# Kernel tuning notes

Measured on AMD Instinct MI355X. Metric: run time of the kernel, lower is better.

Reference implementation:

```python
import jax, jax.numpy as jnp
import numpy as np

D_MODEL = 1024
N_HEADS = 16
D_K = D_MODEL // N_HEADS
SEQ = 4096
BATCH = 1
THETA = 10000.0


def setup_inputs() -> dict:
    key = jax.random.key(0)
    ks = jax.random.split(key, 5)
    scale = 0.02
    x = jax.random.normal(ks[0], (BATCH, SEQ, D_MODEL), dtype=jnp.float32)
    token_positions = jnp.broadcast_to(jnp.arange(SEQ, dtype=jnp.int64 if jax.config.jax_enable_x64 else jnp.int32)[None, :], (BATCH, SEQ))
    Wq = jax.random.normal(ks[1], (D_MODEL, D_MODEL), dtype=jnp.float32) * scale
    Wk = jax.random.normal(ks[2], (D_MODEL, D_MODEL), dtype=jnp.float32) * scale
    Wv = jax.random.normal(ks[3], (D_MODEL, D_MODEL), dtype=jnp.float32) * scale
    Wo = jax.random.normal(ks[4], (D_MODEL, D_MODEL), dtype=jnp.float32) * scale
    return {"x": x, "token_positions": token_positions, "Wq": Wq, "Wk": Wk, "Wv": Wv, "Wo": Wo}


def _apply_rope(t, token_positions, theta=THETA):
    # t: (b, h, s, d_k); token_positions: (b, s)
    d_k = t.shape[-1]
    inv_freq = theta ** (-jnp.arange(0, d_k, 2, dtype=jnp.float32) / d_k)  # (d_k/2,)
    ang = token_positions.astype(jnp.float32)[:, :, None] * inv_freq  # (b, s, d_k/2)
    cos = jnp.cos(ang)[:, None, :, :]  # (b, 1, s, d_k/2)
    sin = jnp.sin(ang)[:, None, :, :]
    te, to = t[..., 0::2], t[..., 1::2]
    re = te * cos - to * sin
    ro = te * sin + to * cos
    # interleave back: (..., d_k/2, 2) -> (..., d_k)
    return jnp.stack([re, ro], axis=-1).reshape(t.shape)


def reference(x, token_positions, Wq, Wk, Wv, Wo):
    b, s, d_model = x.shape
    h, d_k = N_HEADS, D_K
    q = (x @ Wq.T).reshape(b, s, h, d_k).transpose(0, 2, 1, 3)  # (b,h,s,d_k)
    k = (x @ Wk.T).reshape(b, s, h, d_k).transpose(0, 2, 1, 3)
    v = (x @ Wv.T).reshape(b, s, h, d_k).transpose(0, 2, 1, 3)
    q = _apply_rope(q, token_positions)
    k = _apply_rope(k, token_positions)
    scores = jnp.einsum('bhqd,bhkd->bhqk', q, k) / jnp.sqrt(jnp.float32(d_k))
    causal = jnp.tril(jnp.ones((s, s), dtype=bool))[None, None]
    scores = jnp.where(causal, scores, jnp.float32(-1e9))
    attn = jax.nn.softmax(scores, axis=-1)
    out = jnp.einsum('bhqk,bhkd->bhqd', attn, v)  # (b,h,s,d_k)
    out = out.transpose(0, 2, 1, 3).reshape(b, s, d_model)
    return out @ Wo.T
```

## Files before the change

kernel.cpp:

```cpp
#include <hip/hip_runtime.h>
#include <hip/hip_bf16.h>
#include <math.h>


#define SEQ 4096
#define DM  1024
#define NH  16
#define DK  64

typedef __attribute__((ext_vector_type(8))) short short8;
typedef __attribute__((ext_vector_type(4))) float floatx4;

static __device__ __forceinline__ short f2bf(float f) {
    __hip_bfloat16 h = __float2bfloat16(f);
    return __builtin_bit_cast(short, h);
}

static __device__ __forceinline__ short8 load8_f32_as_bf16(const float* p) {
    float4 a = *reinterpret_cast<const float4*>(p);
    float4 b = *reinterpret_cast<const float4*>(p + 4);
    short8 s;
    s[0] = f2bf(a.x); s[1] = f2bf(a.y); s[2] = f2bf(a.z); s[3] = f2bf(a.w);
    s[4] = f2bf(b.x); s[5] = f2bf(b.y); s[6] = f2bf(b.z); s[7] = f2bf(b.w);
    return s;
}

static __device__ __forceinline__ void gl2lds16(const __hip_bfloat16* g, short* l) {
    __builtin_amdgcn_global_load_lds(
        (const __attribute__((address_space(1))) unsigned int*)g,
        (__attribute__((address_space(3))) unsigned int*)l, 16, 0, 0);
}

static __device__ __forceinline__ int read_pos(const int* tp32, int s) {
    return (tp32[1] == 1) ? tp32[s] : tp32[2 * s];
}

__global__ __launch_bounds__(256) void cvt_kernel(
    const float* __restrict__ src, __hip_bfloat16* __restrict__ dst, int n8)
{
    int i = blockIdx.x * blockDim.x + threadIdx.x;
    if (i < n8) {
        short8 v = load8_f32_as_bf16(src + (size_t)i * 8);
        *reinterpret_cast<short8*>((short*)dst + (size_t)i * 8) = v;
    }
}

__global__ __launch_bounds__(256) void rope_tab_kernel(
    const int* __restrict__ tp, float2* __restrict__ tab)
{
    int idx = blockIdx.x * blockDim.x + threadIdx.x;
    if (idx < SEQ * 32) {
        int s = idx >> 5, pair = idx & 31;
        float inv_freq = exp2f(-(float)(2 * pair) * (13.287712379549449f / 64.f));
        float sn, cs;
        sincosf((float)read_pos(tp, s) * inv_freq, &sn, &cs);
        tab[idx] = make_float2(cs, sn);
    }
}

__global__ __launch_bounds__(256) void qkv_rope_kernel(
    const __hip_bfloat16* __restrict__ xb,
    const float2* __restrict__ tab,
    const __hip_bfloat16* __restrict__ Wqb,
    const __hip_bfloat16* __restrict__ Wkb,
    const __hip_bfloat16* __restrict__ Wvb,
    __hip_bfloat16* __restrict__ q_ws,
    __hip_bfloat16* __restrict__ k_ws,
    __hip_bfloat16* __restrict__ vt_ws)
{
    __shared__ __align__(16) short pool[17408];
    short* As = pool;
    short* Bs = pool + 8192;

    const int by = blockIdx.y;
    const int wsel = by >> 3;
    const __hip_bfloat16* W = (wsel == 0) ? Wqb : (wsel == 1 ? Wkb : Wvb);
    const int nloc0 = (by & 7) * 128;
    const int m0 = blockIdx.x * 128;

    const int t = threadIdx.x;
    const int lane = t & 63;
    const int w = t >> 6;
    const int quad = lane >> 4;
    const int ln = lane & 15;
    const int wm = (w >> 1) * 64;
    const int wn = (w & 1) * 64;

    floatx4 acc[4][4];
    #pragma unroll
    for (int i = 0; i < 4; i++)
        #pragma unroll
        for (int j = 0; j < 4; j++) acc[i][j] = (floatx4){0.f, 0.f, 0.f, 0.f};

    for (int k0 = 0; k0 < DM; k0 += 64) {
        #pragma unroll
        for (int it = 0; it < 4; it++) {
            int row = w * 32 + it * 8 + (lane >> 3);
            int sg = (lane & 7) ^ (row & 7);
            gl2lds16(&xb[(size_t)(m0 + row) * DM + k0 + sg * 8], &As[(w * 32 + it * 8) * 64]);
            gl2lds16(&W[(size_t)(nloc0 + row) * DM + k0 + sg * 8], &Bs[(w * 32 + it * 8) * 64]);
        }
        __syncthreads();

        short8 af[4][2], bfr[4][2];
        #pragma unroll
        for (int i = 0; i < 4; i++)
            #pragma unroll
            for (int kc = 0; kc < 2; kc++)
                af[i][kc] = *reinterpret_cast<const short8*>(
                    &As[(wm + i * 16 + ln) * 64 + (((kc * 4 + quad) ^ (ln & 7)) << 3)]);
        #pragma unroll
        for (int j = 0; j < 4; j++)
            #pragma unroll
            for (int kc = 0; kc < 2; kc++)
                bfr[j][kc] = *reinterpret_cast<const short8*>(
                    &Bs[(wn + j * 16 + ln) * 64 + (((kc * 4 + quad) ^ (ln & 7)) << 3)]);

        #pragma unroll
        for (int kc = 0; kc < 2; kc++)
            #pragma unroll
            for (int i = 0; i < 4; i++)
                #pragma unroll
                for (int j = 0; j < 4; j++)
                    acc[i][j] = __builtin_amdgcn_mfma_f32_16x16x32_bf16(
                        af[i][kc], bfr[j][kc], acc[i][j], 0, 0, 0);
        __syncthreads();
    }

    if (wsel < 2) {
        __hip_bfloat16* dst = (wsel == 0) ? q_ws : k_ws;
        const float qscale = (wsel == 0) ? 0.125f : 1.0f;
        #pragma unroll
        for (int j = 0; j < 4; j++) {
            int cnl = wn + j * 16 + ln;
            int pair = ((nloc0 + cnl) & 63) >> 1;
            #pragma unroll
            for (int i = 0; i < 4; i++) {
                int rowl = wm + i * 16 + quad * 4;
                #pragma unroll
                for (int r = 0; r < 4; r++) {
                    float2 t2 = tab[(size_t)(m0 + rowl + r) * 32 + pair];
                    float val = acc[i][j][r];
                    float partner = __shfl_xor(val, 1, 64);
                    float res = val * t2.x + (((lane & 1) ? partner : -partner) * t2.y);
                    pool[(rowl + r) * 136 + cnl] = f2bf(res * qscale);
                }
            }
        }
        __syncthreads();
        int row = t >> 1, half = t & 1;
        size_t gbase = (size_t)(m0 + row) * DM + nloc0 + half * 64;
        #pragma unroll
        for (int c = 0; c < 8; c++)
            *reinterpret_cast<short8*>(&dst[gbase + c * 8]) =
                *reinterpret_cast<const short8*>(&pool[row * 136 + half * 64 + c * 8]);
    } else {
        #pragma unroll
        for (int j = 0; j < 4; j++) {
            int cnl = wn + j * 16 + ln;
            #pragma unroll
            for (int i = 0; i < 4; i++) {
                int s0 = wm + i * 16 + quad * 4;
                #pragma unroll
                for (int r = 0; r < 4; r++)
                    pool[cnl * 136 + s0 + r] = f2bf(acc[i][j][r]);
            }
        }
        __syncthreads();
        int cnl = t >> 1, sh = t & 1;
        size_t base = (size_t)(nloc0 + cnl) * SEQ + m0 + sh * 64;
        #pragma unroll
        for (int c = 0; c < 8; c++)
            *reinterpret_cast<short8*>(&vt_ws[base + c * 8]) =
                *reinterpret_cast<const short8*>(&pool[cnl * 136 + sh * 64 + c * 8]);
    }
}

__global__ __launch_bounds__(512) void attn_kernel(
    const __hip_bfloat16* __restrict__ q_ws,
    const __hip_bfloat16* __restrict__ k_ws,
    const __hip_bfloat16* __restrict__ vt_ws,
    __hip_bfloat16* __restrict__ o_ws)
{
    __shared__ __align__(16) short Kt[2][64 * 64];
    __shared__ __align__(16) short Vt[2][64 * 64];
    __shared__ short P[8][16 * 72];

    const int head = blockIdx.y;
    const int bx = blockIdx.x;
    const int qbA0 = (31 - bx) * 128;
    const int qbB0 = bx * 128;
    const int t = threadIdx.x;
    const int lane = t & 63;
    const int w = t >> 6;
    const int quad = lane >> 4;
    const int ln = lane & 15;
    const int niter = qbA0 / 64 + 2;

    const int qAbase = qbA0 + w * 16;
    const int qBbase = qbB0 + w * 16;

    const int keyl = w * 8 + (lane >> 3);
    const int sg = (lane & 7) ^ (keyl & 7);

    auto stage = [&](int b, int kb) {
        gl2lds16(&k_ws[(size_t)(kb + keyl) * DM + head * 64 + sg * 8], &Kt[b][w * 512]);
        gl2lds16(&vt_ws[(size_t)(head * 64 + keyl) * SEQ + kb + sg * 8], &Vt[b][w * 512]);
    };

    short8 qfA[2], qfB[2];
    #pragma unroll
    for (int kk = 0; kk < 2; kk++) {
        qfA[kk] = *reinterpret_cast<const short8*>(
            &q_ws[(size_t)(qAbase + ln) * DM + head * 64 + kk * 32 + quad * 8]);
        qfB[kk] = *reinterpret_cast<const short8*>(
            &q_ws[(size_t)(qBbase + ln) * DM + head * 64 + kk * 32 + quad * 8]);
    }

    floatx4 accA[4], accB[4];
    float lA[4] = {0.f, 0.f, 0.f, 0.f}, lB[4] = {0.f, 0.f, 0.f, 0.f};
    #pragma unroll
    for (int nt = 0; nt < 4; nt++) {
        accA[nt] = (floatx4){0.f, 0.f, 0.f, 0.f};
        accB[nt] = (floatx4){0.f, 0.f, 0.f, 0.f};
    }
    const floatx4 zero4 = {0.f, 0.f, 0.f, 0.f};

    stage(0, 0);
    int buf = 0;
    for (int it = 0; it < niter; it++) {
        const int kb = it * 64;
        __syncthreads();
        if (it + 1 < niter) stage(buf ^ 1, kb + 64);

        short8 kf[4][2], vf[4][2];
        #pragma unroll
        for (int nt = 0; nt < 4; nt++)
            #pragma unroll
            for (int kk = 0; kk < 2; kk++) {
                kf[nt][kk] = *reinterpret_cast<const short8*>(
                    &Kt[buf][(nt * 16 + ln) * 64 + (((kk * 4 + quad) ^ (ln & 7)) << 3)]);
                vf[nt][kk] = *reinterpret_cast<const short8*>(
                    &Vt[buf][(nt * 16 + ln) * 64 + (((kk * 4 + quad) ^ (ln & 7)) << 3)]);
            }

        if (kb <= qAbase + 15) {
            floatx4 sacc[4];
            #pragma unroll
            for (int nt = 0; nt < 4; nt++) {
                floatx4 s = __builtin_amdgcn_mfma_f32_16x16x32_bf16(qfA[0], kf[nt][0], zero4, 0, 0, 0);
                sacc[nt] = __builtin_amdgcn_mfma_f32_16x16x32_bf16(qfA[1], kf[nt][1], s, 0, 0, 0);
            }
            if (kb + 63 > qAbase) {
                #pragma unroll
                for (int nt = 0; nt < 4; nt++) {
                    int kpos = kb + nt * 16 + ln;
                    #pragma unroll
                    for (int r = 0; r < 4; r++)
                        if (kpos > qAbase + quad * 4 + r) sacc[nt][r] = -1e9f;
                }
            }
            #pragma unroll
            for (int nt = 0; nt < 4; nt++)
                #pragma unroll
                for (int r = 0; r < 4; r++) {
                    float p = __expf(sacc[nt][r]);
                    sacc[nt][r] = p;
                    lA[r] += p;
                }
            #pragma unroll
            for (int nt = 0; nt < 4; nt++)
                #pragma unroll
                for (int r = 0; r < 4; r++)
                    P[w][(quad * 4 + r) * 72 + nt * 16 + ln] = f2bf(sacc[nt][r]);
            short8 pa[2];
            #pragma unroll
            for (int kk = 0; kk < 2; kk++)
                pa[kk] = *reinterpret_cast<const short8*>(&P[w][ln * 72 + kk * 32 + quad * 8]);
            #pragma unroll
            for (int nt = 0; nt < 4; nt++) {
                floatx4 o = __builtin_amdgcn_mfma_f32_16x16x32_bf16(pa[0], vf[nt][0], accA[nt], 0, 0, 0);
                accA[nt] = __builtin_amdgcn_mfma_f32_16x16x32_bf16(pa[1], vf[nt][1], o, 0, 0, 0);
            }
        }
        if (kb <= qBbase + 15) {
            floatx4 sacc[4];
            #pragma unroll
            for (int nt = 0; nt < 4; nt++) {
                floatx4 s = __builtin_amdgcn_mfma_f32_16x16x32_bf16(qfB[0], kf[nt][0], zero4, 0, 0, 0);
                sacc[nt] = __builtin_amdgcn_mfma_f32_16x16x32_bf16(qfB[1], kf[nt][1], s, 0, 0, 0);
            }
            if (kb + 63 > qBbase) {
                #pragma unroll
                for (int nt = 0; nt < 4; nt++) {
                    int kpos = kb + nt * 16 + ln;
                    #pragma unroll
                    for (int r = 0; r < 4; r++)
                        if (kpos > qBbase + quad * 4 + r) sacc[nt][r] = -1e9f;
                }
            }
            #pragma unroll
            for (int nt = 0; nt < 4; nt++)
                #pragma unroll
                for (int r = 0; r < 4; r++) {
                    float p = __expf(sacc[nt][r]);
                    sacc[nt][r] = p;
                    lB[r] += p;
                }
            #pragma unroll
            for (int nt = 0; nt < 4; nt++)
                #pragma unroll
                for (int r = 0; r < 4; r++)
                    P[w][(quad * 4 + r) * 72 + nt * 16 + ln] = f2bf(sacc[nt][r]);
            short8 pa[2];
            #pragma unroll
            for (int kk = 0; kk < 2; kk++)
                pa[kk] = *reinterpret_cast<const short8*>(&P[w][ln * 72 + kk * 32 + quad * 8]);
            #pragma unroll
            for (int nt = 0; nt < 4; nt++) {
                floatx4 o = __builtin_amdgcn_mfma_f32_16x16x32_bf16(pa[0], vf[nt][0], accB[nt], 0, 0, 0);
                accB[nt] = __builtin_amdgcn_mfma_f32_16x16x32_bf16(pa[1], vf[nt][1], o, 0, 0, 0);
            }
        }
        buf ^= 1;
    }

    #pragma unroll
    for (int r = 0; r < 4; r++) {
        float l = lA[r];
        #pragma unroll
        for (int off = 1; off < 16; off <<= 1)
            l += __shfl_xor(l, off, 64);
        float rl = 1.f / l;
        int row = qAbase + quad * 4 + r;
        #pragma unroll
        for (int nt = 0; nt < 4; nt++)
            o_ws[(size_t)row * DM + head * 64 + nt * 16 + ln] =
                __float2bfloat16(accA[nt][r] * rl);
    }
    #pragma unroll
    for (int r = 0; r < 4; r++) {
        float l = lB[r];
        #pragma unroll
        for (int off = 1; off < 16; off <<= 1)
            l += __shfl_xor(l, off, 64);
        float rl = 1.f / l;
        int row = qBbase + quad * 4 + r;
        #pragma unroll
        for (int nt = 0; nt < 4; nt++)
            o_ws[(size_t)row * DM + head * 64 + nt * 16 + ln] =
                __float2bfloat16(accB[nt][r] * rl);
    }
}

__global__ __launch_bounds__(256) void oproj_kernel(
    const __hip_bfloat16* __restrict__ o_in,
    const float* __restrict__ Wo,
    float* __restrict__ out)
{
    __shared__ __align__(16) char smem[33792];
    short* As = (short*)smem;
    short* Bs = As + 8192;
    float* fpool = (float*)smem;

    const int m0 = blockIdx.x * 128;
    const int n0 = blockIdx.y * 128;

    const int t = threadIdx.x;
    const int lane = t & 63;
    const int w = t >> 6;
    const int quad = lane >> 4;
    const int ln = lane & 15;
    const int wm = (w >> 1) * 64;
    const int wn = (w & 1) * 64;

    floatx4 acc[4][4];
    #pragma unroll
    for (int i = 0; i < 4; i++)
        #pragma unroll
        for (int j = 0; j < 4; j++) acc[i][j] = (floatx4){0.f, 0.f, 0.f, 0.f};

    for (int k0 = 0; k0 < DM; k0 += 64) {
        #pragma unroll
        for (int it = 0; it < 4; it++) {
            int row = w * 32 + it * 8 + (lane >> 3);
            int sg = (lane & 7) ^ (row & 7);
            gl2lds16(&o_in[(size_t)(m0 + row) * DM + k0 + sg * 8], &As[(w * 32 + it * 8) * 64]);
        }
        #pragma unroll
        for (int p = 0; p < 4; p++) {
            int r = (t >> 3) + p * 32;
            int sg = t & 7;
            *reinterpret_cast<short8*>(&Bs[r * 64 + ((sg ^ (r & 7)) << 3)]) =
                load8_f32_as_bf16(&Wo[(size_t)(n0 + r) * DM + k0 + sg * 8]);
        }
        __syncthreads();

        short8 af[4][2], bfr[4][2];
        #pragma unroll
        for (int i = 0; i < 4; i++)
            #pragma unroll
            for (int kc = 0; kc < 2; kc++)
                af[i][kc] = *reinterpret_cast<const short8*>(
                    &As[(wm + i * 16 + ln) * 64 + (((kc * 4 + quad) ^ (ln & 7)) << 3)]);
        #pragma unroll
        for (int j = 0; j < 4; j++)
            #pragma unroll
            for (int kc = 0; kc < 2; kc++)
                bfr[j][kc] = *reinterpret_cast<const short8*>(
                    &Bs[(wn + j * 16 + ln) * 64 + (((kc * 4 + quad) ^ (ln & 7)) << 3)]);

        #pragma unroll
        for (int kc = 0; kc < 2; kc++)
            #pragma unroll
            for (int i = 0; i < 4; i++)
                #pragma unroll
                for (int j = 0; j < 4; j++)
                    acc[i][j] = __builtin_amdgcn_mfma_f32_16x16x32_bf16(
                        af[i][kc], bfr[j][kc], acc[i][j], 0, 0, 0);
        __syncthreads();
    }

    #pragma unroll
    for (int ph = 0; ph < 2; ph++) {
        if ((w >> 1) == ph) {
            #pragma unroll
            for (int j = 0; j < 4; j++)
                #pragma unroll
                for (int i = 0; i < 4; i++) {
                    int rl = i * 16 + quad * 4;
                    #pragma unroll
                    for (int r = 0; r < 4; r++)
                        fpool[(rl + r) * 132 + wn + j * 16 + ln] = acc[i][j][r];
                }
        }
        __syncthreads();
        int row = t >> 2;
        int c0 = (t & 3) * 32;
        size_t gbase = (size_t)(m0 + ph * 64 + row) * DM + n0 + c0;
        #pragma unroll
        for (int c = 0; c < 8; c++)
            *reinterpret_cast<float4*>(&out[gbase + c * 4]) =
                *reinterpret_cast<const float4*>(&fpool[row * 132 + c0 + c * 4]);
        __syncthreads();
    }
}

extern "C" void kernel_launch(void* const* d_in, const int* in_sizes, int n_in,
                              void* d_out, int out_size, void* d_ws, size_t ws_size,
                              hipStream_t stream) {
    const float* x  = (const float*)d_in[0];
    const int* tp   = (const int*)d_in[1];
    const float* Wq = (const float*)d_in[2];
    const float* Wk = (const float*)d_in[3];
    const float* Wv = (const float*)d_in[4];
    const float* Wo = (const float*)d_in[5];
    float* out = (float*)d_out;

    char* ws = (char*)d_ws;
    const size_t MB = 1024 * 1024;
    __hip_bfloat16* xb    = (__hip_bfloat16*)(ws);
    __hip_bfloat16* q_ws  = (__hip_bfloat16*)(ws + 8  * MB);
    __hip_bfloat16* k_ws  = (__hip_bfloat16*)(ws + 16 * MB);
    __hip_bfloat16* vt_ws = (__hip_bfloat16*)(ws + 24 * MB);
    __hip_bfloat16* o_ws  = xb;
    __hip_bfloat16* Wqb = (__hip_bfloat16*)d_out;
    __hip_bfloat16* Wkb = Wqb + (size_t)DM * DM;
    __hip_bfloat16* Wvb = Wkb + (size_t)DM * DM;
    float2* tab = (float2*)((char*)d_out + 6 * MB);

    cvt_kernel<<<2048, 256, 0, stream>>>(x,  xb,  (SEQ * DM) / 8);
    cvt_kernel<<<512,  256, 0, stream>>>(Wq, Wqb, (DM * DM) / 8);
    cvt_kernel<<<512,  256, 0, stream>>>(Wk, Wkb, (DM * DM) / 8);
    cvt_kernel<<<512,  256, 0, stream>>>(Wv, Wvb, (DM * DM) / 8);
    rope_tab_kernel<<<(SEQ * 32 + 255) / 256, 256, 0, stream>>>(tp, tab);

    qkv_rope_kernel<<<dim3(32, 24), 256, 0, stream>>>(xb, tab, Wqb, Wkb, Wvb, q_ws, k_ws, vt_ws);
    attn_kernel<<<dim3(16, 16), 512, 0, stream>>>(q_ws, k_ws, vt_ws, o_ws);
    oproj_kernel<<<dim3(32, 8), 256, 0, stream>>>(o_ws, Wo, out);
}
```

Baseline: 252.4 us.

## Fuse prep launches and transpose attention score MFMA for packed P stores

Merges the four fp32-to-bf16 conversion launches and the RoPE table launch into a single prep kernel, removing four kernel launches and their inter-launch gaps. In the attention kernel, the score MFMA operands are swapped so each lane holds four consecutive keys for one query. This allows P to be written to shared memory as packed 4-element stores into an XOR-swizzled, unpadded layout, and reduces the row-sum to one scalar per lane. The risk is a different LDS bank pattern and some extra shuffles in the epilogue.

Result: faster. 235.1 us (-6.9%).

```diff
diff --git a/kernel.cpp b/kernel.cpp
--- a/kernel.cpp
+++ b/kernel.cpp
@@ -10,6 +10,7 @@
 
 typedef __attribute__((ext_vector_type(8))) short short8;
 typedef __attribute__((ext_vector_type(4))) float floatx4;
+typedef __attribute__((ext_vector_type(4))) short short4v;
 
 static __device__ __forceinline__ short f2bf(float f) {
     __hip_bfloat16 h = __float2bfloat16(f);
@@ -35,26 +36,33 @@
     return (tp32[1] == 1) ? tp32[s] : tp32[2 * s];
 }
 
-__global__ __launch_bounds__(256) void cvt_kernel(
-    const float* __restrict__ src, __hip_bfloat16* __restrict__ dst, int n8)
+__global__ __launch_bounds__(256) void prep_kernel(
+    const float* __restrict__ x,  const float* __restrict__ Wq,
+    const float* __restrict__ Wk, const float* __restrict__ Wv,
+    const int* __restrict__ tp,
+    __hip_bfloat16* __restrict__ xb,  __hip_bfloat16* __restrict__ Wqb,
+    __hip_bfloat16* __restrict__ Wkb, __hip_bfloat16* __restrict__ Wvb,
+    float2* __restrict__ tab)
 {
-    int i = blockIdx.x * blockDim.x + threadIdx.x;
-    if (i < n8) {
-        short8 v = load8_f32_as_bf16(src + (size_t)i * 8);
-        *reinterpret_cast<short8*>((short*)dst + (size_t)i * 8) = v;
-    }
-}
-
-__global__ __launch_bounds__(256) void rope_tab_kernel(
-    const int* __restrict__ tp, float2* __restrict__ tab)
-{
-    int idx = blockIdx.x * blockDim.x + threadIdx.x;
-    if (idx < SEQ * 32) {
-        int s = idx >> 5, pair = idx & 31;
-        float inv_freq = exp2f(-(float)(2 * pair) * (13.287712379549449f / 64.f));
-        float sn, cs;
-        sincosf((float)read_pos(tp, s) * inv_freq, &sn, &cs);
-        tab[idx] = make_float2(cs, sn);
+    int b = blockIdx.x;
+    if (b < 3584) {
+        const float* src; __hip_bfloat16* dst; int off;
+        if (b < 2048)      { src = x;  dst = xb;  off = b; }
+        else if (b < 2560) { src = Wq; dst = Wqb; off = b - 2048; }
+        else if (b < 3072) { src = Wk; dst = Wkb; off = b - 2560; }
+        else               { src = Wv; dst = Wvb; off = b - 3072; }
+        size_t i = (size_t)off * 256 + threadIdx.x;
+        short8 v = load8_f32_as_bf16(src + i * 8);
+        *reinterpret_cast<short8*>((short*)dst + i * 8) = v;
+    } else {
+        int idx = (b - 3584) * 256 + threadIdx.x;
+        if (idx < SEQ * 32) {
+            int s = idx >> 5, pair = idx & 31;
+            float inv_freq = exp2f(-(float)(2 * pair) * (13.287712379549449f / 64.f));
+            float sn, cs;
+            sincosf((float)read_pos(tp, s) * inv_freq, &sn, &cs);
+            tab[idx] = make_float2(cs, sn);
+        }
     }
 }
 
@@ -184,7 +192,7 @@
 {
     __shared__ __align__(16) short Kt[2][64 * 64];
     __shared__ __align__(16) short Vt[2][64 * 64];
-    __shared__ short P[8][16 * 72];
+    __shared__ __align__(16) short P[8][16 * 64];
 
     const int head = blockIdx.y;
     const int bx = blockIdx.x;
@@ -195,10 +203,11 @@
     const int w = t >> 6;
     const int quad = lane >> 4;
     const int ln = lane & 15;
-    const int niter = qbA0 / 64 + 2;
+    const int niter = (31 - bx) * 2 + 2;
 
     const int qAbase = qbA0 + w * 16;
     const int qBbase = qbB0 + w * 16;
+    const int e = ((ln & 7) << 1) ^ (ln & 8);
 
     const int keyl = w * 8 + (lane >> 3);
     const int sg = (lane & 7) ^ (keyl & 7);
@@ -218,7 +227,7 @@
     }
 
     floatx4 accA[4], accB[4];
-    float lA[4] = {0.f, 0.f, 0.f, 0.f}, lB[4] = {0.f, 0.f, 0.f, 0.f};
+    float lA = 0.f, lB = 0.f;
     #pragma unroll
     for (int nt = 0; nt < 4; nt++) {
         accA[nt] = (floatx4){0.f, 0.f, 0.f, 0.f};
@@ -248,16 +257,17 @@
             floatx4 sacc[4];
             #pragma unroll
             for (int nt = 0; nt < 4; nt++) {
-                floatx4 s = __builtin_amdgcn_mfma_f32_16x16x32_bf16(qfA[0], kf[nt][0], zero4, 0, 0, 0);
-                sacc[nt] = __builtin_amdgcn_mfma_f32_16x16x32_bf16(qfA[1], kf[nt][1], s, 0, 0, 0);
-            }
+                floatx4 s = __builtin_amdgcn_mfma_f32_16x16x32_bf16(kf[nt][0], qfA[0], zero4, 0, 0, 0);
+                sacc[nt] = __builtin_amdgcn_mfma_f32_16x16x32_bf16(kf[nt][1], qfA[1], s, 0, 0, 0);
+            }
+            const int qpos = qAbase + ln;
             if (kb + 63 > qAbase) {
                 #pragma unroll
                 for (int nt = 0; nt < 4; nt++) {
-                    int kpos = kb + nt * 16 + ln;
+                    int kbase = kb + nt * 16 + quad * 4;
                     #pragma unroll
                     for (int r = 0; r < 4; r++)
-                        if (kpos > qAbase + quad * 4 + r) sacc[nt][r] = -1e9f;
+                        if (kbase + r > qpos) sacc[nt][r] = -1e9f;
                 }
             }
             #pragma unroll
@@ -266,17 +276,19 @@
                 for (int r = 0; r < 4; r++) {
                     float p = __expf(sacc[nt][r]);
                     sacc[nt][r] = p;
-                    lA[r] += p;
-                }
-            #pragma unroll
-            for (int nt = 0; nt < 4; nt++)
-                #pragma unroll
-                for (int r = 0; r < 4; r++)
-                    P[w][(quad * 4 + r) * 72 + nt * 16 + ln] = f2bf(sacc[nt][r]);
+                    lA += p;
+                }
+            #pragma unroll
+            for (int nt = 0; nt < 4; nt++) {
+                short4v pk = { f2bf(sacc[nt][0]), f2bf(sacc[nt][1]),
+                               f2bf(sacc[nt][2]), f2bf(sacc[nt][3]) };
+                *reinterpret_cast<short4v*>(&P[w][ln * 64 + (((nt * 4 + quad) ^ e) << 2)]) = pk;
+            }
             short8 pa[2];
             #pragma unroll
             for (int kk = 0; kk < 2; kk++)
-                pa[kk] = *reinterpret_cast<const short8*>(&P[w][ln * 72 + kk * 32 + quad * 8]);
+                pa[kk] = *reinterpret_cast<const short8*>(
+                    &P[w][ln * 64 + (((kk * 8 + quad * 2) ^ e) << 2)]);
             #pragma unroll
             for (int nt = 0; nt < 4; nt++) {
                 floatx4 o = __builtin_amdgcn_mfma_f32_16x16x32_bf16(pa[0], vf[nt][0], accA[nt], 0, 0, 0);
@@ -287,16 +299,17 @@
             floatx4 sacc[4];
             #pragma unroll
             for (int nt = 0; nt < 4; nt++) {
-                floatx4 s = __builtin_amdgcn_mfma_f32_16x16x32_bf16(qfB[0], kf[nt][0], zero4, 0, 0, 0);
-                sacc[nt] = __builtin_amdgcn_mfma_f32_16x16x32_bf16(qfB[1], kf[nt][1], s, 0, 0, 0);
-            }
+                floatx4 s = __builtin_amdgcn_mfma_f32_16x16x32_bf16(kf[nt][0], qfB[0], zero4, 0, 0, 0);
+                sacc[nt] = __builtin_amdgcn_mfma_f32_16x16x32_bf16(kf[nt][1], qfB[1], s, 0, 0, 0);
+            }
+            const int qpos = qBbase + ln;
             if (kb + 63 > qBbase) {
                 #pragma unroll
                 for (int nt = 0; nt < 4; nt++) {
-                    int kpos = kb + nt * 16 + ln;
+                    int kbase = kb + nt * 16 + quad * 4;
                     #pragma unroll
                     for (int r = 0; r < 4; r++)
-                        if (kpos > qBbase + quad * 4 + r) sacc[nt][r] = -1e9f;
+                        if (kbase + r > qpos) sacc[nt][r] = -1e9f;
                 }
             }
             #pragma unroll
@@ -305,17 +318,19 @@
                 for (int r = 0; r < 4; r++) {
                     float p = __expf(sacc[nt][r]);
                     sacc[nt][r] = p;
-                    lB[r] += p;
-                }
-            #pragma unroll
-            for (int nt = 0; nt < 4; nt++)
-                #pragma unroll
-                for (int r = 0; r < 4; r++)
-                    P[w][(quad * 4 + r) * 72 + nt * 16 + ln] = f2bf(sacc[nt][r]);
+                    lB += p;
+                }
+            #pragma unroll
+            for (int nt = 0; nt < 4; nt++) {
+                short4v pk = { f2bf(sacc[nt][0]), f2bf(sacc[nt][1]),
+                               f2bf(sacc[nt][2]), f2bf(sacc[nt][3]) };
+                *reinterpret_cast<short4v*>(&P[w][ln * 64 + (((nt * 4 + quad) ^ e) << 2)]) = pk;
+            }
             short8 pa[2];
             #pragma unroll
             for (int kk = 0; kk < 2; kk++)
-                pa[kk] = *reinterpret_cast<const short8*>(&P[w][ln * 72 + kk * 32 + quad * 8]);
+                pa[kk] = *reinterpret_cast<const short8*>(
+                    &P[w][ln * 64 + (((kk * 8 + quad * 2) ^ e) << 2)]);
             #pragma unroll
             for (int nt = 0; nt < 4; nt++) {
                 floatx4 o = __builtin_amdgcn_mfma_f32_16x16x32_bf16(pa[0], vf[nt][0], accB[nt], 0, 0, 0);
@@ -325,31 +340,33 @@
         buf ^= 1;
     }
 
-    #pragma unroll
-    for (int r = 0; r < 4; r++) {
-        float l = lA[r];
-        #pragma unroll
-        for (int off = 1; off < 16; off <<= 1)
-            l += __shfl_xor(l, off, 64);
-        float rl = 1.f / l;
-        int row = qAbase + quad * 4 + r;
-        #pragma unroll
-        for (int nt = 0; nt < 4; nt++)
-            o_ws[(size_t)row * DM + head * 64 + nt * 16 + ln] =
-                __float2bfloat16(accA[nt][r] * rl);
-    }
-    #pragma unroll
-    for (int r = 0; r < 4; r++) {
-        float l = lB[r];
-        #pragma unroll
-        for (int off = 1; off < 16; off <<= 1)
-            l += __shfl_xor(l, off, 64);
-        float rl = 1.f / l;
-        int row = qBbase + quad * 4 + r;
-        #pragma unroll
-        for (int nt = 0; nt < 4; nt++)
-            o_ws[(size_t)row * DM + head * 64 + nt * 16 + ln] =
-                __float2bfloat16(accB[nt][r] * rl);
+    {
+        float l = lA;
+        l += __shfl_xor(l, 16, 64);
+        l += __shfl_xor(l, 32, 64);
+        #pragma unroll
+        for (int r = 0; r < 4; r++) {
+            float rl = 1.f / __shfl(l, quad * 4 + r, 64);
+            int row = qAbase + quad * 4 + r;
+            #pragma unroll
+            for (int nt = 0; nt < 4; nt++)
+                o_ws[(size_t)row * DM + head * 64 + nt * 16 + ln] =
+                    __float2bfloat16(accA[nt][r] * rl);
+        }
+    }
+    {
+        float l = lB;
+        l += __shfl_xor(l, 16, 64);
+        l += __shfl_xor(l, 32, 64);
+        #pragma unroll
+        for (int r = 0; r < 4; r++) {
+            float rl = 1.f / __shfl(l, quad * 4 + r, 64);
+            int row = qBbase + quad * 4 + r;
+            #pragma unroll
+            for (int nt = 0; nt < 4; nt++)
+                o_ws[(size_t)row * DM + head * 64 + nt * 16 + ln] =
+                    __float2bfloat16(accB[nt][r] * rl);
+        }
     }
 }
 
@@ -390,9 +407,9 @@
         #pragma unroll
         for (int p = 0; p < 4; p++) {
             int r = (t >> 3) + p * 32;
-            int sg = t & 7;
-            *reinterpret_cast<short8*>(&Bs[r * 64 + ((sg ^ (r & 7)) << 3)]) =
-                load8_f32_as_bf16(&Wo[(size_t)(n0 + r) * DM + k0 + sg * 8]);
+            int sg2 = t & 7;
+            *reinterpret_cast<short8*>(&Bs[r * 64 + ((sg2 ^ (r & 7)) << 3)]) =
+                load8_f32_as_bf16(&Wo[(size_t)(n0 + r) * DM + k0 + sg2 * 8]);
         }
         __syncthreads();
 
@@ -469,12 +486,7 @@
     __hip_bfloat16* Wvb = Wkb + (size_t)DM * DM;
     float2* tab = (float2*)((char*)d_out + 6 * MB);
 
-    cvt_kernel<<<2048, 256, 0, stream>>>(x,  xb,  (SEQ * DM) / 8);
-    cvt_kernel<<<512,  256, 0, stream>>>(Wq, Wqb, (DM * DM) / 8);
-    cvt_kernel<<<512,  256, 0, stream>>>(Wk, Wkb, (DM * DM) / 8);
-    cvt_kernel<<<512,  256, 0, stream>>>(Wv, Wvb, (DM * DM) / 8);
-    rope_tab_kernel<<<(SEQ * 32 + 255) / 256, 256, 0, stream>>>(tp, tab);
-
+    prep_kernel<<<4096, 256, 0, stream>>>(x, Wq, Wk, Wv, tp, xb, Wqb, Wkb, Wvb, tab);
     qkv_rope_kernel<<<dim3(32, 24), 256, 0, stream>>>(xb, tab, Wqb, Wkb, Wvb, q_ws, k_ws, vt_ws);
     attn_kernel<<<dim3(16, 16), 512, 0, stream>>>(q_ws, k_ws, vt_ws, o_ws);
     oproj_kernel<<<dim3(32, 8), 256, 0, stream>>>(o_ws, Wo, out);
```
